# Performance work log

Hardware: AMD Instinct MI355X
Metric: run time of the kernel (lower is better)

The kernel has to match this reference:

```python
import jax, jax.numpy as jnp
import numpy as np

B, T, D = 1, 4096, 768
H, HD = 12, 64  # num_heads, head_dim; H*HD == D


def setup_inputs() -> dict:
    key = jax.random.key(0)
    ks = jax.random.split(key, 12)
    s = 1.0 / np.sqrt(D)  # nn.Linear-style init scale
    inp = {
        "query": jax.random.normal(ks[0], (B, T, D), jnp.float32),
        "key": jax.random.normal(ks[1], (B, T, D), jnp.float32),
        "value": jax.random.normal(ks[2], (B, T, D), jnp.float32),
        # causal mask: True positions are masked (strict upper triangle)
        "mask": jnp.triu(jnp.ones((T, T), dtype=bool), k=1),
        "Wq_w": jax.random.normal(ks[3], (D, D), jnp.float32) * s,
        "Wq_b": jax.random.normal(ks[4], (D,), jnp.float32) * s,
        "Wk_w": jax.random.normal(ks[5], (D, D), jnp.float32) * s,
        "Wk_b": jax.random.normal(ks[6], (D,), jnp.float32) * s,
        "Wv_w": jax.random.normal(ks[7], (D, D), jnp.float32) * s,
        "Wv_b": jax.random.normal(ks[8], (D,), jnp.float32) * s,
        "W0_w": jax.random.normal(ks[9], (D, D), jnp.float32) * s,
        "W0_b": jax.random.normal(ks[10], (D,), jnp.float32) * s,
    }
    return inp


def _split_heads(x):
    # (B, T, D) -> (B, H, T, HD)
    b, t, _ = x.shape
    return x.reshape(b, t, H, HD).transpose(0, 2, 1, 3)


def reference(query, key, value, mask, Wq_w, Wq_b, Wk_w, Wk_b, Wv_w, Wv_b, W0_w, W0_b):
    # Q/K/V projections (torch Linear: x @ W.T + b)
    q = _split_heads(query @ Wq_w.T + Wq_b)
    k = _split_heads(key @ Wk_w.T + Wk_b)
    v = _split_heads(value @ Wv_w.T + Wv_b)

    scale = 1.0 / jnp.sqrt(jnp.asarray(HD, q.dtype))
    scores = jnp.einsum("bhqd,bhkd->bhqk", q, k) * scale  # (B,H,T,T)
    scores = jnp.where(mask, -jnp.inf, scores)
    weights = jax.nn.softmax(scores, axis=-1)  # (B,H,T,T)
    attn = jnp.einsum("bhqk,bhkd->bhqd", weights, v)  # (B,H,T,HD)

    # concat heads: (B,H,T,HD) -> (B,T,D), then output projection
    out = attn.transpose(0, 2, 1, 3).reshape(query.shape[0], -1, D)
    output = out @ W0_w.T + W0_b
    return output, weights
```

## Files before the change

### kernel.cpp

```cpp
#include <hip/hip_runtime.h>

#define TSEQ 4096
#define DM 768
#define NHEAD 12
#define HDIM 64
#define SC 0.1803368801111204f

using f32x4  = __attribute__((ext_vector_type(4))) float;
using bf16x8 = __attribute__((ext_vector_type(8))) short;
using bf16x4 = __attribute__((ext_vector_type(4))) short;

__device__ __forceinline__ short f2bf(float f) {
    union { float f; unsigned u; } x; x.f = f;
    unsigned r = x.u + 0x7FFFu + ((x.u >> 16) & 1u);
    return (short)(r >> 16);
}

__device__ __forceinline__ f32x4 mfma16(bf16x8 a, bf16x8 b, f32x4 c) {
    return __builtin_amdgcn_mfma_f32_16x16x32_bf16(a, b, c, 0, 0, 0);
}

__global__ __launch_bounds__(256) void gemm_qkv(
    const float* __restrict__ q_in, const float* __restrict__ k_in,
    const float* __restrict__ v_in,
    const float* __restrict__ Wq_w, const float* __restrict__ Wq_b,
    const float* __restrict__ Wk_w, const float* __restrict__ Wk_b,
    const float* __restrict__ Wv_w, const float* __restrict__ Wv_b,
    short* __restrict__ Qb, short* __restrict__ Kb, short* __restrict__ Vt)
{
    constexpr int K = DM;
    __shared__ __align__(16) short As[64 * 72];
    __shared__ __align__(16) short Bs[64 * 72];
    const int z = blockIdx.z;
    const float* A    = (z == 0) ? q_in : (z == 1) ? k_in : v_in;
    const float* W    = (z == 0) ? Wq_w : (z == 1) ? Wk_w : Wv_w;
    const float* bias = (z == 0) ? Wq_b : (z == 1) ? Wk_b : Wv_b;

    const int bm = blockIdx.x * 64;
    const int bn = blockIdx.y * 64;
    const int tid = threadIdx.x;
    const int wid = tid >> 6;
    const int lane = tid & 63;
    const int l15 = lane & 15, lq = lane >> 4;

    f32x4 acc[4] = {};
    const int sr = tid >> 3;
    const int sc = (tid & 7) * 8;

    for (int k0 = 0; k0 < K; k0 += 64) {
        #pragma unroll
        for (int it = 0; it < 2; ++it) {
            int r = sr + it * 32;
            const float* ga = A + (size_t)(bm + r) * K + k0 + sc;
            f32x4 a0 = *(const f32x4*)ga;
            f32x4 a1 = *(const f32x4*)(ga + 4);
            bf16x8 av;
            #pragma unroll
            for (int j = 0; j < 4; ++j) { av[j] = f2bf(a0[j]); av[4 + j] = f2bf(a1[j]); }
            *(bf16x8*)&As[r * 72 + sc] = av;
            const float* gb = W + (size_t)(bn + r) * K + k0 + sc;
            f32x4 b0 = *(const f32x4*)gb;
            f32x4 b1 = *(const f32x4*)(gb + 4);
            bf16x8 bv;
            #pragma unroll
            for (int j = 0; j < 4; ++j) { bv[j] = f2bf(b0[j]); bv[4 + j] = f2bf(b1[j]); }
            *(bf16x8*)&Bs[r * 72 + sc] = bv;
        }
        __syncthreads();
        __builtin_amdgcn_s_setprio(1);
        #pragma unroll
        for (int ks = 0; ks < 2; ++ks) {
            bf16x8 af = *(bf16x8*)&As[(wid * 16 + l15) * 72 + ks * 32 + lq * 8];
            #pragma unroll
            for (int n = 0; n < 4; ++n) {
                bf16x8 bfv = *(bf16x8*)&Bs[(n * 16 + l15) * 72 + ks * 32 + lq * 8];
                acc[n] = mfma16(af, bfv, acc[n]);
            }
        }
        __builtin_amdgcn_s_setprio(0);
        __syncthreads();
    }

    const int row0 = bm + wid * 16 + lq * 4;
    #pragma unroll
    for (int n = 0; n < 4; ++n) {
        int col = bn + n * 16 + l15;
        float b = bias[col];
        if (z == 2) {
            bf16x4 v;
            #pragma unroll
            for (int r = 0; r < 4; ++r) v[r] = f2bf(acc[n][r] + b);
            *(bf16x4*)(Vt + (size_t)col * TSEQ + row0) = v;
        } else {
            short* dst = (z == 0) ? Qb : Kb;
            #pragma unroll
            for (int r = 0; r < 4; ++r)
                dst[(size_t)(row0 + r) * DM + col] = f2bf(acc[n][r] + b);
        }
    }
}

__global__ __launch_bounds__(256) void gemm_out(
    const float* __restrict__ A, const float* __restrict__ W,
    const float* __restrict__ bias, float* __restrict__ Cout)
{
    constexpr int K = DM;
    __shared__ __align__(16) short As[64 * 72];
    __shared__ __align__(16) short Bs[64 * 72];
    const int bm = blockIdx.x * 64;
    const int bn = blockIdx.y * 64;
    const int tid = threadIdx.x;
    const int wid = tid >> 6;
    const int lane = tid & 63;
    const int l15 = lane & 15, lq = lane >> 4;

    f32x4 acc[4] = {};
    const int sr = tid >> 3;
    const int sc = (tid & 7) * 8;

    for (int k0 = 0; k0 < K; k0 += 64) {
        #pragma unroll
        for (int it = 0; it < 2; ++it) {
            int r = sr + it * 32;
            const float* ga = A + (size_t)(bm + r) * K + k0 + sc;
            f32x4 a0 = *(const f32x4*)ga;
            f32x4 a1 = *(const f32x4*)(ga + 4);
            bf16x8 av;
            #pragma unroll
            for (int j = 0; j < 4; ++j) { av[j] = f2bf(a0[j]); av[4 + j] = f2bf(a1[j]); }
            *(bf16x8*)&As[r * 72 + sc] = av;
            const float* gb = W + (size_t)(bn + r) * K + k0 + sc;
            f32x4 b0 = *(const f32x4*)gb;
            f32x4 b1 = *(const f32x4*)(gb + 4);
            bf16x8 bv;
            #pragma unroll
            for (int j = 0; j < 4; ++j) { bv[j] = f2bf(b0[j]); bv[4 + j] = f2bf(b1[j]); }
            *(bf16x8*)&Bs[r * 72 + sc] = bv;
        }
        __syncthreads();
        __builtin_amdgcn_s_setprio(1);
        #pragma unroll
        for (int ks = 0; ks < 2; ++ks) {
            bf16x8 af = *(bf16x8*)&As[(wid * 16 + l15) * 72 + ks * 32 + lq * 8];
            #pragma unroll
            for (int n = 0; n < 4; ++n) {
                bf16x8 bfv = *(bf16x8*)&Bs[(n * 16 + l15) * 72 + ks * 32 + lq * 8];
                acc[n] = mfma16(af, bfv, acc[n]);
            }
        }
        __builtin_amdgcn_s_setprio(0);
        __syncthreads();
    }

    const int row0 = bm + wid * 16 + lq * 4;
    #pragma unroll
    for (int n = 0; n < 4; ++n) {
        int col = bn + n * 16 + l15;
        float b = bias[col];
        #pragma unroll
        for (int r = 0; r < 4; ++r)
            Cout[(size_t)(row0 + r) * DM + col] = acc[n][r] + b;
    }
}

__global__ __launch_bounds__(256) void attn_fused(
    const short* __restrict__ Qb, const short* __restrict__ Kb,
    const short* __restrict__ Vt, float* __restrict__ Wout,
    float* __restrict__ AttnO)
{
    const int qt = 63 - blockIdx.x;
    const int h = blockIdx.y;
    const int q0 = qt * 64;
    const int tid = threadIdx.x, wid = tid >> 6, lane = tid & 63;
    const int l15 = lane & 15, lq = lane >> 4;

    __shared__ __align__(16) short lds[23040];

    const int nkt = qt + 1;

    {
        float* wbase = Wout + (size_t)h * TSEQ * TSEQ + (size_t)(q0 + wid * 16) * TSEQ;
        f32x4 z = {0.f, 0.f, 0.f, 0.f};
        for (int kt = nkt; kt < 64; ++kt) {
            #pragma unroll
            for (int i = 0; i < 4; ++i)
                *(f32x4*)(wbase + (size_t)(lq + i * 4) * TSEQ + kt * 64 + l15 * 4) = z;
        }
    }

    const short* qp = Qb + (size_t)(q0 + wid * 16 + l15) * DM + h * HDIM + lq * 8;
    bf16x8 qf0 = *(const bf16x8*)qp;
    bf16x8 qf1 = *(const bf16x8*)(qp + 32);

    const short* kbase = Kb + (size_t)h * HDIM;
    const short* vbase = Vt + (size_t)h * HDIM * TSEQ;
    const int myq = q0 + wid * 16 + l15;

    const int srow = tid >> 3;
    const int scol = (tid & 7) * 8;

    const int nch = (nkt + 1) >> 1;
    auto stageKbig = [&](int c, int b) {
        const int base_k = c * 128;
        const int iters = (nkt * 64 - base_k) >= 128 ? 4 : 2;
        short* dst = lds + b * (128 * 72);
        for (int it = 0; it < iters; ++it) {
            int r = srow + it * 32;
            *(bf16x8*)&dst[r * 72 + scol] =
                *(const bf16x8*)&kbase[(size_t)(base_k + r) * DM + scol];
        }
    };

    f32x4 lacc = {0.f, 0.f, 0.f, 0.f};
    stageKbig(0, 0);
    __syncthreads();
    for (int c = 0; c < nch; ++c) {
        const int b = c & 1;
        if (c + 1 < nch) stageKbig(c + 1, b ^ 1);
        const short* kb = lds + b * (128 * 72);
        #pragma unroll
        for (int t = 0; t < 2; ++t) {
            const int kt = c * 2 + t;
            if (kt >= nkt) break;
            f32x4 s[4] = {};
            __builtin_amdgcn_s_setprio(1);
            #pragma unroll
            for (int ks = 0; ks < 2; ++ks) {
                bf16x8 qf = ks ? qf1 : qf0;
                #pragma unroll
                for (int n = 0; n < 4; ++n) {
                    bf16x8 kf = *(const bf16x8*)
                        &kb[(t * 64 + n * 16 + l15) * 72 + ks * 32 + lq * 8];
                    s[n] = mfma16(kf, qf, s[n]);
                }
            }
            __builtin_amdgcn_s_setprio(0);
            if (kt == qt) {
                #pragma unroll
                for (int n = 0; n < 4; ++n) {
                    int kb0 = kt * 64 + n * 16 + lq * 4;
                    #pragma unroll
                    for (int r = 0; r < 4; ++r)
                        lacc[n] += (kb0 + r <= myq) ? exp2f(s[n][r] * SC) : 0.f;
                }
            } else {
                #pragma unroll
                for (int n = 0; n < 4; ++n)
                    #pragma unroll
                    for (int r = 0; r < 4; ++r)
                        lacc[n] += exp2f(s[n][r] * SC);
            }
        }
        __syncthreads();
    }
    float lsum = (lacc[0] + lacc[1]) + (lacc[2] + lacc[3]);
    lsum += __shfl_xor(lsum, 16);
    lsum += __shfl_xor(lsum, 32);
    const float linv = 1.f / lsum;

    short* Ks2 = lds;
    short* Vs2 = lds + 2 * 64 * 72;
    short* Psw = lds + 4 * 64 * 72 + wid * (16 * 72);

    auto stageK2 = [&](int kt, int b) {
        short* dst = Ks2 + b * (64 * 72);
        #pragma unroll
        for (int it = 0; it < 2; ++it) {
            int r = srow + it * 32;
            *(bf16x8*)&dst[r * 72 + scol] =
                *(const bf16x8*)&kbase[(size_t)(kt * 64 + r) * DM + scol];
        }
    };
    auto stageV2 = [&](int kt, int b) {
        short* dst = Vs2 + b * (64 * 72);
        #pragma unroll
        for (int it = 0; it < 2; ++it) {
            int r = srow + it * 32;
            *(bf16x8*)&dst[r * 72 + scol] =
                *(const bf16x8*)&vbase[(size_t)r * TSEQ + kt * 64 + scol];
        }
    };

    float* wq = Wout + (size_t)h * TSEQ * TSEQ + (size_t)myq * TSEQ;
    f32x4 o[4] = {};
    stageK2(0, 0);
    stageV2(0, 0);
    __syncthreads();
    for (int kt = 0; kt < nkt; ++kt) {
        const int b = kt & 1;
        if (kt + 1 < nkt) { stageK2(kt + 1, b ^ 1); stageV2(kt + 1, b ^ 1); }
        f32x4 s[4] = {};
        __builtin_amdgcn_s_setprio(1);
        #pragma unroll
        for (int ks = 0; ks < 2; ++ks) {
            bf16x8 qf = ks ? qf1 : qf0;
            #pragma unroll
            for (int n = 0; n < 4; ++n) {
                bf16x8 kf = *(const bf16x8*)
                    &Ks2[b * (64 * 72) + (n * 16 + l15) * 72 + ks * 32 + lq * 8];
                s[n] = mfma16(kf, qf, s[n]);
            }
        }
        __builtin_amdgcn_s_setprio(0);
        const bool diag = (kt == qt);
        #pragma unroll
        for (int n = 0; n < 4; ++n) {
            const int kb0 = kt * 64 + n * 16 + lq * 4;
            f32x4 p;
            #pragma unroll
            for (int r = 0; r < 4; ++r) {
                float e = exp2f(s[n][r] * SC) * linv;
                p[r] = (diag && (kb0 + r > myq)) ? 0.f : e;
            }
            *(f32x4*)(wq + kb0) = p;
            bf16x4 pb;
            #pragma unroll
            for (int r = 0; r < 4; ++r) pb[r] = f2bf(p[r]);
            *(bf16x4*)&Psw[l15 * 72 + n * 16 + lq * 4] = pb;
        }
        __builtin_amdgcn_s_setprio(1);
        #pragma unroll
        for (int ks = 0; ks < 2; ++ks) {
            bf16x8 pf = *(bf16x8*)&Psw[l15 * 72 + ks * 32 + lq * 8];
            #pragma unroll
            for (int n = 0; n < 4; ++n) {
                bf16x8 vf = *(const bf16x8*)
                    &Vs2[b * (64 * 72) + (n * 16 + l15) * 72 + ks * 32 + lq * 8];
                o[n] = mfma16(pf, vf, o[n]);
            }
        }
        __builtin_amdgcn_s_setprio(0);
        __syncthreads();
    }

    #pragma unroll
    for (int n = 0; n < 4; ++n) {
        int col = h * HDIM + n * 16 + l15;
        #pragma unroll
        for (int r = 0; r < 4; ++r) {
            int row = q0 + wid * 16 + lq * 4 + r;
            AttnO[(size_t)row * DM + col] = o[n][r];
        }
    }
}

extern "C" void kernel_launch(void* const* d_in, const int* in_sizes, int n_in,
                              void* d_out, int out_size, void* d_ws, size_t ws_size,
                              hipStream_t stream)
{
    const float* q_in = (const float*)d_in[0];
    const float* k_in = (const float*)d_in[1];
    const float* v_in = (const float*)d_in[2];
    const float* Wq_w = (const float*)d_in[4];
    const float* Wq_b = (const float*)d_in[5];
    const float* Wk_w = (const float*)d_in[6];
    const float* Wk_b = (const float*)d_in[7];
    const float* Wv_w = (const float*)d_in[8];
    const float* Wv_b = (const float*)d_in[9];
    const float* W0_w = (const float*)d_in[10];
    const float* W0_b = (const float*)d_in[11];

    float* out  = (float*)d_out;
    float* wout = out + (size_t)TSEQ * DM;

    short* Qb = (short*)d_ws;
    short* Kb = Qb + (size_t)TSEQ * DM;
    short* Vt = Kb + (size_t)TSEQ * DM;
    float* AttnO = (float*)(Vt + (size_t)TSEQ * DM);

    gemm_qkv<<<dim3(TSEQ / 64, DM / 64, 3), 256, 0, stream>>>(
        q_in, k_in, v_in, Wq_w, Wq_b, Wk_w, Wk_b, Wv_w, Wv_b, Qb, Kb, Vt);
    attn_fused<<<dim3(64, NHEAD), 256, 0, stream>>>(Qb, Kb, Vt, wout, AttnO);
    gemm_out<<<dim3(TSEQ / 64, DM / 64), 256, 0, stream>>>(AttnO, W0_w, W0_b, out);
}
```

Baseline: 370.3 us.

## Prefetch K/V into registers, use nontemporal weight stores and lighter barriers

In the second attention pass, the next K/V tile is now loaded from global memory into registers before the compute and written to LDS only after it, so load latency overlaps with the MFMA and softmax work. Stores of the large attention-weight matrix, including the zero-filled masked region, become nontemporal to reduce cache pollution. __syncthreads is replaced by an explicit s_waitcnt lgkmcnt(0) plus s_barrier that does not wait on outstanding vector memory ops. The inline-asm barrier bypasses the compiler's own wait insertion and relies on it still waiting correctly for global loads before the LDS writes, and register prefetch raises register pressure.

Measured after the change: 342.7 us. -7.5%, faster.

```diff
diff --git a/kernel.cpp b/kernel.cpp
--- a/kernel.cpp
+++ b/kernel.cpp
@@ -9,6 +9,8 @@
 using f32x4  = __attribute__((ext_vector_type(4))) float;
 using bf16x8 = __attribute__((ext_vector_type(8))) short;
 using bf16x4 = __attribute__((ext_vector_type(4))) short;
+
+#define LGKM_BARRIER() asm volatile("s_waitcnt lgkmcnt(0)\n\ts_barrier" ::: "memory")
 
 __device__ __forceinline__ short f2bf(float f) {
     union { float f; unsigned u; } x; x.f = f;
@@ -66,7 +68,7 @@
             for (int j = 0; j < 4; ++j) { bv[j] = f2bf(b0[j]); bv[4 + j] = f2bf(b1[j]); }
             *(bf16x8*)&Bs[r * 72 + sc] = bv;
         }
-        __syncthreads();
+        LGKM_BARRIER();
         __builtin_amdgcn_s_setprio(1);
         #pragma unroll
         for (int ks = 0; ks < 2; ++ks) {
@@ -78,7 +80,7 @@
             }
         }
         __builtin_amdgcn_s_setprio(0);
-        __syncthreads();
+        LGKM_BARRIER();
     }
 
     const int row0 = bm + wid * 16 + lq * 4;
@@ -137,7 +139,7 @@
             for (int j = 0; j < 4; ++j) { bv[j] = f2bf(b0[j]); bv[4 + j] = f2bf(b1[j]); }
             *(bf16x8*)&Bs[r * 72 + sc] = bv;
         }
-        __syncthreads();
+        LGKM_BARRIER();
         __builtin_amdgcn_s_setprio(1);
         #pragma unroll
         for (int ks = 0; ks < 2; ++ks) {
@@ -149,7 +151,7 @@
             }
         }
         __builtin_amdgcn_s_setprio(0);
-        __syncthreads();
+        LGKM_BARRIER();
     }
 
     const int row0 = bm + wid * 16 + lq * 4;
@@ -184,7 +186,8 @@
         for (int kt = nkt; kt < 64; ++kt) {
             #pragma unroll
             for (int i = 0; i < 4; ++i)
-                *(f32x4*)(wbase + (size_t)(lq + i * 4) * TSEQ + kt * 64 + l15 * 4) = z;
+                __builtin_nontemporal_store(
+                    z, (f32x4*)(wbase + (size_t)(lq + i * 4) * TSEQ + kt * 64 + l15 * 4));
         }
     }
 
@@ -213,7 +216,7 @@
 
     f32x4 lacc = {0.f, 0.f, 0.f, 0.f};
     stageKbig(0, 0);
-    __syncthreads();
+    LGKM_BARRIER();
     for (int c = 0; c < nch; ++c) {
         const int b = c & 1;
         if (c + 1 < nch) stageKbig(c + 1, b ^ 1);
@@ -251,7 +254,7 @@
                         lacc[n] += exp2f(s[n][r] * SC);
             }
         }
-        __syncthreads();
+        LGKM_BARRIER();
     }
     float lsum = (lacc[0] + lacc[1]) + (lacc[2] + lacc[3]);
     lsum += __shfl_xor(lsum, 16);
@@ -262,33 +265,34 @@
     short* Vs2 = lds + 2 * 64 * 72;
     short* Psw = lds + 4 * 64 * 72 + wid * (16 * 72);
 
-    auto stageK2 = [&](int kt, int b) {
-        short* dst = Ks2 + b * (64 * 72);
-        #pragma unroll
-        for (int it = 0; it < 2; ++it) {
-            int r = srow + it * 32;
-            *(bf16x8*)&dst[r * 72 + scol] =
-                *(const bf16x8*)&kbase[(size_t)(kt * 64 + r) * DM + scol];
-        }
+    bf16x8 krg0, krg1, vrg0, vrg1;
+    auto loadKV = [&](int kt) {
+        krg0 = *(const bf16x8*)&kbase[(size_t)(kt * 64 + srow) * DM + scol];
+        krg1 = *(const bf16x8*)&kbase[(size_t)(kt * 64 + srow + 32) * DM + scol];
+        vrg0 = *(const bf16x8*)&vbase[(size_t)srow * TSEQ + kt * 64 + scol];
+        vrg1 = *(const bf16x8*)&vbase[(size_t)(srow + 32) * TSEQ + kt * 64 + scol];
     };
-    auto stageV2 = [&](int kt, int b) {
-        short* dst = Vs2 + b * (64 * 72);
-        #pragma unroll
-        for (int it = 0; it < 2; ++it) {
-            int r = srow + it * 32;
-            *(bf16x8*)&dst[r * 72 + scol] =
-                *(const bf16x8*)&vbase[(size_t)r * TSEQ + kt * 64 + scol];
-        }
+    auto writeKV = [&](int b) {
+        short* kd = Ks2 + b * (64 * 72);
+        short* vd = Vs2 + b * (64 * 72);
+        *(bf16x8*)&kd[srow * 72 + scol] = krg0;
+        *(bf16x8*)&kd[(srow + 32) * 72 + scol] = krg1;
+        *(bf16x8*)&vd[srow * 72 + scol] = vrg0;
+        *(bf16x8*)&vd[(srow + 32) * 72 + scol] = vrg1;
     };
 
     float* wq = Wout + (size_t)h * TSEQ * TSEQ + (size_t)myq * TSEQ;
     f32x4 o[4] = {};
-    stageK2(0, 0);
-    stageV2(0, 0);
-    __syncthreads();
+    loadKV(0);
+    writeKV(0);
+    LGKM_BARRIER();
     for (int kt = 0; kt < nkt; ++kt) {
         const int b = kt & 1;
-        if (kt + 1 < nkt) { stageK2(kt + 1, b ^ 1); stageV2(kt + 1, b ^ 1); }
+        const bool more = (kt + 1 < nkt);
+        if (more) {
+            loadKV(kt + 1);
+            __builtin_amdgcn_sched_barrier(0);
+        }
         f32x4 s[4] = {};
         __builtin_amdgcn_s_setprio(1);
         #pragma unroll
@@ -312,7 +316,7 @@
                 float e = exp2f(s[n][r] * SC) * linv;
                 p[r] = (diag && (kb0 + r > myq)) ? 0.f : e;
             }
-            *(f32x4*)(wq + kb0) = p;
+            __builtin_nontemporal_store(p, (f32x4*)(wq + kb0));
             bf16x4 pb;
             #pragma unroll
             for (int r = 0; r < 4; ++r) pb[r] = f2bf(p[r]);
@@ -330,7 +334,11 @@
             }
         }
         __builtin_amdgcn_s_setprio(0);
-        __syncthreads();
+        if (more) {
+            __builtin_amdgcn_sched_barrier(0);
+            writeKV(b ^ 1);
+        }
+        LGKM_BARRIER();
     }
 
     #pragma unroll
```
